# Optimization experiments

Hardware: AMD Instinct MI355X
Metric: run time of the kernel (lower is better)

## Reference

```python
import jax, jax.numpy as jnp
import numpy as np

EPS = 1e-8

def mlp(x, w1, b1, w2, b2):
    return jnp.tanh(x @ w1 + b1) @ w2 + b2

def setup_inputs() -> dict:
    key = jax.random.key(0)
    ks = jax.random.split(key, 24)
    N_NEWS, N_USERS, N_ATR = 50000, 100000, 1000
    E_ATR, E_USR = 100000, 2000000
    D = 768
    def lin(k, fi, fo):
        return jax.random.normal(k, (fi, fo), jnp.float32) * (1.0 / np.sqrt(fi))
    inp = {
        'news_x': jax.random.normal(ks[0], (N_NEWS, D), jnp.float32),
        'users_x': jax.random.normal(ks[1], (N_USERS, 128), jnp.float32),
        'w1a': lin(ks[2], D, 256), 'b1a': jnp.zeros((256,), jnp.float32),
        'w1b': lin(ks[3], 256, 128), 'b1b': jnp.zeros((128,), jnp.float32),
        'wna': lin(ks[4], D + 128, 512), 'bna': jnp.zeros((512,), jnp.float32),
        'wnb': lin(ks[5], 512, 128), 'bnb': jnp.zeros((128,), jnp.float32),
        'wua': lin(ks[6], 256, 256), 'bua': jnp.zeros((256,), jnp.float32),
        'wub': lin(ks[7], 256, 128), 'bub': jnp.zeros((128,), jnp.float32),
        'atr_row': jax.random.randint(ks[8], (E_ATR,), 0, N_NEWS, jnp.int32),
        'atr_col': jax.random.randint(ks[9], (E_ATR,), 0, N_ATR, jnp.int32),
        'usr_row': jax.random.randint(ks[10], (E_USR,), 0, N_NEWS, jnp.int32),
        'usr_col': jax.random.randint(ks[11], (E_USR,), 0, N_USERS, jnp.int32),
        'n_news': N_NEWS, 'n_users': N_USERS, 'n_atr': N_ATR,
    }
    return inp

def reference(news_x, users_x, w1a, b1a, w1b, b1b, wna, bna, wnb, bnb,
              wua, bua, wub, bub, atr_row, atr_col, usr_row, usr_col,
              n_news, n_users, n_atr):
    dt = news_x.dtype
    ones_a = jnp.ones(atr_row.shape[0], dt)
    ones_u = jnp.ones(usr_row.shape[0], dt)
    # FirstConv: news -> attribute nodes (edge_index.t() @ news)
    deg_atr = jax.ops.segment_sum(ones_a, atr_col, num_segments=n_atr)
    agr_atr = jax.ops.segment_sum(news_x[atr_row], atr_col, num_segments=n_atr)
    agr_atr = agr_atr / (deg_atr[:, None] + EPS)
    atr_feats = mlp(agr_atr, w1a, b1a, w1b, b1b)  # [n_atr, 128]
    # NewsConv: attribute -> news (edge_index @ atr_feats), concat with news_x
    deg_news = jax.ops.segment_sum(ones_a, atr_row, num_segments=n_news)
    agr_news = jax.ops.segment_sum(atr_feats[atr_col], atr_row, num_segments=n_news)
    agr_news = agr_news / (deg_news[:, None] + EPS)
    news_out = mlp(jnp.concatenate([news_x, agr_news], axis=1), wna, bna, wnb, bnb)  # [n_news,128]
    # UserConv: news -> users (edge_index['users'].t() @ news), concat with users_x
    deg_usr = jax.ops.segment_sum(ones_u, usr_col, num_segments=n_users)
    agr_usr = jax.ops.segment_sum(news_out[usr_row], usr_col, num_segments=n_users)
    agr_usr = agr_usr / (deg_usr[:, None] + EPS)
    users_out = mlp(jnp.concatenate([users_x, agr_usr], axis=1), wua, bua, wub, bub)  # [n_users,128]
    # stack final news + user embeddings into one array
    return jnp.concatenate([news_out, users_out], axis=0)  # [n_news+n_users, 128]
```

## Files before the change

### kernel.cpp

```cpp
#include <hip/hip_runtime.h>

#define N_NEWS 50000
#define N_USERS 100000
#define N_ATR 1000
#define E_ATR 100000
#define E_USR 2000000
#define EPSF 1e-8f

#define ACAP 192
#define NCAP 24
#define P_USR 250
#define UPP 400
#define ACAPP 9216
#define EBLK_A 4096

typedef short s16x8 __attribute__((ext_vector_type(8)));
typedef float f32x4 __attribute__((ext_vector_type(4)));

__device__ inline ushort f2bf(float f) {
    uint u = __float_as_uint(f);
    u += 0x7fffu + ((u >> 16) & 1u);
    return (ushort)(u >> 16);
}
__device__ inline float bflo(uint v) { return __uint_as_float(v << 16); }
__device__ inline float bfhi(uint v) { return __uint_as_float(v & 0xffff0000u); }
__device__ inline float fast_tanh(float x) {
    x = fminf(fmaxf(x, -15.0f), 15.0f);
    float e = __expf(2.0f * x);
    return (e - 1.0f) / (e + 1.0f);
}

struct TrJob { const float* src; ushort* dst; int R, C, blkEnd; };

struct PrepArgs {
    const int *atr_row, *atr_col, *usr_row, *usr_col;
    int *cnt_atr, *cnt_news, *arena_cnt;
    int *ids_atr, *ids_news;
    unsigned long long* arena;
    const float *news_x, *users_x;
    ushort *news_bf, *users_bf;
    int pa, fa, tr, n1, n2;
    TrJob j[6];
};

__global__ void prep_k(PrepArgs A) {
    __shared__ float tile[32][33];
    __shared__ int cloc[256], cscn[256], sexc[256], cbase[256];
    __shared__ ushort stageI[EBLK_A];
    int b = blockIdx.x;
    int t = threadIdx.x;
    if (b < A.pa) {
        cloc[t] = 0;
        __syncthreads();
        int base = b * EBLK_A;
        int endE = base + EBLK_A; if (endE > E_USR) endE = E_USR;
        int n = endE - base;
        for (int e = base + t; e < endE; e += 256)
            atomicAdd(&cloc[A.usr_col[e] / UPP], 1);
        __syncthreads();
        cscn[t] = cloc[t];
        __syncthreads();
        for (int off = 1; off < 256; off <<= 1) {
            int v = (t >= off) ? cscn[t - off] : 0;
            __syncthreads();
            cscn[t] += v;
            __syncthreads();
        }
        sexc[t] = cscn[t] - cloc[t];
        if (t < P_USR) cbase[t] = atomicAdd(&A.arena_cnt[t], cloc[t]);
        cloc[t] = 0;
        __syncthreads();
        for (int e = base + t; e < endE; e += 256) {
            int p = A.usr_col[e] / UPP;
            int off = atomicAdd(&cloc[p], 1);
            stageI[sexc[p] + off] = (ushort)(e - base);
        }
        __syncthreads();
        for (int i = t; i < n; i += 256) {
            int e = base + stageI[i];
            int c = A.usr_col[e];
            int r = A.usr_row[e];
            int p = c / UPP;
            int dst = cbase[p] + (i - sexc[p]);
            if (dst < ACAPP)
                A.arena[(size_t)p * ACAPP + dst] =
                    ((unsigned long long)(uint)c << 32) | (uint)r;
        }
        return;
    }
    b -= A.pa;
    if (b < A.fa) {
        int total = 2 * E_ATR;
        int per = (total + A.fa - 1) / A.fa;
        int base = b * per;
        int endE = base + per; if (endE > total) endE = total;
        for (int e = base + t; e < endE; e += 256) {
            if (e < E_ATR) {
                int c = A.atr_col[e];
                int slot = atomicAdd(&A.cnt_atr[c], 1);
                if (slot < ACAP) A.ids_atr[(size_t)c * ACAP + slot] = A.atr_row[e];
            } else {
                int e2 = e - E_ATR;
                int r = A.atr_row[e2];
                int slot = atomicAdd(&A.cnt_news[r], 1);
                if (slot < NCAP) A.ids_news[(size_t)r * NCAP + slot] = A.atr_col[e2];
            }
        }
        return;
    }
    b -= A.fa;
    if (b < A.tr) {
        int ji = 0;
        while (b >= A.j[ji].blkEnd) ++ji;
        const TrJob& J = A.j[ji];
        int lb = b - (ji ? A.j[ji - 1].blkEnd : 0);
        int ctiles = J.C / 32;
        int bc = (lb % ctiles) * 32, br = (lb / ctiles) * 32;
        int tx = t & 31, ty = t >> 5;
        for (int i = 0; i < 4; ++i)
            tile[ty + i * 8][tx] = J.src[(size_t)(br + ty + i * 8) * J.C + bc + tx];
        __syncthreads();
        for (int i = 0; i < 4; ++i)
            J.dst[(size_t)(bc + ty + i * 8) * J.R + br + tx] = f2bf(tile[tx][ty + i * 8]);
        return;
    }
    b -= A.tr;
    int i = b * 256 + t;
    const float* src; ushort* dst;
    if (i < A.n1) { src = A.news_x; dst = A.news_bf; }
    else          { i -= A.n1; if (i >= A.n2) return; src = A.users_x; dst = A.users_bf; }
    float4 a = ((const float4*)src)[i];
    uint2 v;
    v.x = (uint)f2bf(a.x) | ((uint)f2bf(a.y) << 16);
    v.y = (uint)f2bf(a.z) | ((uint)f2bf(a.w) << 16);
    ((uint2*)dst)[i] = v;
}

struct MidArgs {
    const unsigned long long* arena;
    const int* arena_cnt;
    int *cnt_usr, *start_usr, *ids_usr;
    const ushort* news_bf;
    const int* ids_atr;
    const int* cnt_atr;
    ushort* agr_atr_b;
};

__global__ void mid_k(MidArgs M) {
    __shared__ int cnt[512];
    __shared__ int scn[512];
    int b = blockIdx.x;
    int t = threadIdx.x;
    if (b < P_USR) {
        int p = b;
        int nA = M.arena_cnt[p]; if (nA > ACAPP) nA = ACAPP;
        const unsigned long long* ar = M.arena + (size_t)p * ACAPP;
        cnt[t] = 0; cnt[t + 256] = 0;
        __syncthreads();
        for (int i = t; i < nA; i += 256)
            atomicAdd(&cnt[(int)(ar[i] >> 32) - p * UPP], 1);
        __syncthreads();
        scn[t] = cnt[t]; scn[t + 256] = cnt[t + 256];
        __syncthreads();
        for (int off = 1; off < 512; off <<= 1) {
            int v0 = (t >= off) ? scn[t - off] : 0;
            int v1 = ((t + 256) >= off) ? scn[t + 256 - off] : 0;
            __syncthreads();
            scn[t] += v0; scn[t + 256] += v1;
            __syncthreads();
        }
        for (int i = t; i < UPP; i += 256) {
            int u = p * UPP + i;
            M.cnt_usr[u] = cnt[i];
            M.start_usr[u] = p * ACAPP + (scn[i] - cnt[i]);
        }
        __syncthreads();
        for (int i = t; i < UPP; i += 256) cnt[i] = scn[i] - cnt[i];
        __syncthreads();
        for (int i = t; i < nA; i += 256) {
            unsigned long long v = ar[i];
            int c = (int)(v >> 32);
            int off = atomicAdd(&cnt[c - p * UPP], 1);
            M.ids_usr[(size_t)p * ACAPP + off] = (int)(v & 0xffffffffu);
        }
        return;
    }
    b -= P_USR;
    int u = b;
    int dc = M.cnt_atr[u];
    int d = dc < ACAP ? dc : ACAP;
    const int* bp = M.ids_atr + (size_t)u * ACAP;
    const ushort* src = M.news_bf;
    float a0 = 0.f, a1 = 0.f, a2 = 0.f, a3 = 0.f;
    int i = 0;
    for (; i + 3 < d; i += 4) {
        const uint* r0 = (const uint*)(src + (size_t)bp[i] * 768);
        const uint* r1 = (const uint*)(src + (size_t)bp[i + 1] * 768);
        const uint* r2 = (const uint*)(src + (size_t)bp[i + 2] * 768);
        const uint* r3 = (const uint*)(src + (size_t)bp[i + 3] * 768);
        uint v0 = r0[t], v1 = r1[t], v2 = r2[t], v3 = r3[t];
        a0 += bflo(v0) + bflo(v1) + bflo(v2) + bflo(v3);
        a1 += bfhi(v0) + bfhi(v1) + bfhi(v2) + bfhi(v3);
        if (t < 128) {
            uint w0 = r0[t + 256], w1 = r1[t + 256], w2 = r2[t + 256], w3 = r3[t + 256];
            a2 += bflo(w0) + bflo(w1) + bflo(w2) + bflo(w3);
            a3 += bfhi(w0) + bfhi(w1) + bfhi(w2) + bfhi(w3);
        }
    }
    for (; i < d; ++i) {
        const uint* r0 = (const uint*)(src + (size_t)bp[i] * 768);
        uint v0 = r0[t];
        a0 += bflo(v0); a1 += bfhi(v0);
        if (t < 128) {
            uint v1 = r0[t + 256];
            a2 += bflo(v1); a3 += bfhi(v1);
        }
    }
    float inv = 1.0f / ((float)dc + EPSF);
    uint* dst = (uint*)(M.agr_atr_b + (size_t)u * 768);
    dst[t] = (uint)f2bf(a0 * inv) | ((uint)f2bf(a1 * inv) << 16);
    if (t < 128)
        dst[256 + t] = (uint)f2bf(a2 * inv) | ((uint)f2bf(a3 * inv) << 16);
}

template<int CAP>
__global__ void gather128c_k(const ushort* __restrict__ srcp, const int* __restrict__ ids,
                             const int* __restrict__ cnt, ushort* __restrict__ agr, int n) {
    int u = blockIdx.x * 8 + (threadIdx.x >> 5);
    if (u >= n) return;
    int lane = threadIdx.x & 31;
    int dc = cnt[u];
    int d = dc < CAP ? dc : CAP;
    const int* bp = ids + (size_t)u * CAP;
    float a0 = 0.f, a1 = 0.f, a2 = 0.f, a3 = 0.f;
    int i = 0;
    for (; i + 3 < d; i += 4) {
        int s0 = bp[i], s1 = bp[i + 1], s2 = bp[i + 2], s3 = bp[i + 3];
        uint2 v0 = *((const uint2*)(srcp + (size_t)s0 * 128) + lane);
        uint2 v1 = *((const uint2*)(srcp + (size_t)s1 * 128) + lane);
        uint2 v2 = *((const uint2*)(srcp + (size_t)s2 * 128) + lane);
        uint2 v3 = *((const uint2*)(srcp + (size_t)s3 * 128) + lane);
        a0 += bflo(v0.x) + bflo(v1.x) + bflo(v2.x) + bflo(v3.x);
        a1 += bfhi(v0.x) + bfhi(v1.x) + bfhi(v2.x) + bfhi(v3.x);
        a2 += bflo(v0.y) + bflo(v1.y) + bflo(v2.y) + bflo(v3.y);
        a3 += bfhi(v0.y) + bfhi(v1.y) + bfhi(v2.y) + bfhi(v3.y);
    }
    for (; i < d; ++i) {
        uint2 v0 = *((const uint2*)(srcp + (size_t)bp[i] * 128) + lane);
        a0 += bflo(v0.x); a1 += bfhi(v0.x);
        a2 += bflo(v0.y); a3 += bfhi(v0.y);
    }
    float inv = 1.0f / ((float)dc + EPSF);
    uint2 packed;
    packed.x = (uint)f2bf(a0 * inv) | ((uint)f2bf(a1 * inv) << 16);
    packed.y = (uint)f2bf(a2 * inv) | ((uint)f2bf(a3 * inv) << 16);
    *((uint2*)(agr + (size_t)u * 128) + lane) = packed;
}

__global__ void gather128s_k(const ushort* __restrict__ srcp, const int* __restrict__ ids,
                             const int* __restrict__ start, const int* __restrict__ cnt,
                             ushort* __restrict__ agr, int n) {
    int u = blockIdx.x * 8 + (threadIdx.x >> 5);
    if (u >= n) return;
    int lane = threadIdx.x & 31;
    int d = cnt[u];
    const int* bp = ids + start[u];
    float a0 = 0.f, a1 = 0.f, a2 = 0.f, a3 = 0.f;
    int i = 0;
    for (; i + 3 < d; i += 4) {
        int s0 = bp[i], s1 = bp[i + 1], s2 = bp[i + 2], s3 = bp[i + 3];
        uint2 v0 = *((const uint2*)(srcp + (size_t)s0 * 128) + lane);
        uint2 v1 = *((const uint2*)(srcp + (size_t)s1 * 128) + lane);
        uint2 v2 = *((const uint2*)(srcp + (size_t)s2 * 128) + lane);
        uint2 v3 = *((const uint2*)(srcp + (size_t)s3 * 128) + lane);
        a0 += bflo(v0.x) + bflo(v1.x) + bflo(v2.x) + bflo(v3.x);
        a1 += bfhi(v0.x) + bfhi(v1.x) + bfhi(v2.x) + bfhi(v3.x);
        a2 += bflo(v0.y) + bflo(v1.y) + bflo(v2.y) + bflo(v3.y);
        a3 += bfhi(v0.y) + bfhi(v1.y) + bfhi(v2.y) + bfhi(v3.y);
    }
    for (; i < d; ++i) {
        uint2 v0 = *((const uint2*)(srcp + (size_t)bp[i] * 128) + lane);
        a0 += bflo(v0.x); a1 += bfhi(v0.x);
        a2 += bflo(v0.y); a3 += bfhi(v0.y);
    }
    float inv = 1.0f / ((float)d + EPSF);
    uint2 packed;
    packed.x = (uint)f2bf(a0 * inv) | ((uint)f2bf(a1 * inv) << 16);
    packed.y = (uint)f2bf(a2 * inv) | ((uint)f2bf(a3 * inv) << 16);
    *((uint2*)(agr + (size_t)u * 128) + lane) = packed;
}

template<int NS, int NS1, bool TANH, int OMODE, int GY>
__launch_bounds__(256, 3)
__global__ void gemm5_k(const ushort* __restrict__ A1, const ushort* __restrict__ A2,
                        const ushort* __restrict__ Bt, const float* __restrict__ bias,
                        float* __restrict__ outf, ushort* __restrict__ outb,
                        int M, int N) {
    __shared__ __align__(16) char lds[32768];
    const int t = threadIdx.x;
    const int w = t >> 6, l = t & 63, lr = l & 15, lk = l >> 4;
    const int wm = w >> 1, wn = w & 1;
    int nwg = gridDim.x;
    int q = nwg >> 3, r = nwg & 7;
    int xcd = blockIdx.x & 7, idx = blockIdx.x >> 3;
    int fid = (xcd < r) ? xcd * (q + 1) + idx : r * (q + 1) + (xcd - r) * q + idx;
    constexpr int LG = (GY == 4) ? 2 : (GY == 2) ? 1 : 0;
    const int row0 = (fid >> LG) * 128;
    const int col0 = (fid & (GY - 1)) * 128;
    constexpr int A1RB = NS1 * 128;
    constexpr int A2RB = (NS - NS1) * 128;
    constexpr int BRB = NS * 128;

    auto stage = [&](int s) {
        const char* abase; int arb, soff;
        if (s < NS1) { abase = (const char*)A1; arb = A1RB; soff = s * 128; }
        else         { abase = (const char*)A2; arb = A2RB; soff = (s - NS1) * 128; }
#pragma unroll
        for (int i = 0; i < 4; ++i) {
            int chunk = i * 256 + w * 64 + l;
            int row = chunk >> 3, sub = chunk & 7;
            int rg = row0 + row; if (rg >= M) rg = M - 1;
            const char* src = abase + (size_t)rg * arb + soff + ((sub * 16) ^ ((row & 7) << 4));
            __builtin_amdgcn_global_load_lds(
                (const __attribute__((address_space(1))) unsigned int*)src,
                (__attribute__((address_space(3))) unsigned int*)(lds + i * 4096 + w * 1024),
                16, 0, 0);
        }
#pragma unroll
        for (int i = 0; i < 4; ++i) {
            int chunk = i * 256 + w * 64 + l;
            int row = chunk >> 3, sub = chunk & 7;
            const char* src = (const char*)Bt + (size_t)(col0 + row) * BRB + s * 128
                              + ((sub * 16) ^ ((row & 7) << 4));
            __builtin_amdgcn_global_load_lds(
                (const __attribute__((address_space(1))) unsigned int*)src,
                (__attribute__((address_space(3))) unsigned int*)(lds + 16384 + i * 4096 + w * 1024),
                16, 0, 0);
        }
    };

    f32x4 acc[4][4];
#pragma unroll
    for (int i = 0; i < 4; ++i)
#pragma unroll
        for (int j = 0; j < 4; ++j) acc[i][j] = (f32x4)0.f;

    stage(0);
    for (int s = 0; s < NS; ++s) {
        __syncthreads();
#pragma unroll
        for (int ks = 0; ks < 2; ++ks) {
            s16x8 af[4], bf[4];
#pragma unroll
            for (int rt = 0; rt < 4; ++rt) {
                int rr = wm * 64 + rt * 16 + lr;
                af[rt] = *(const s16x8*)(lds + rr * 128 + ((ks * 64 + lk * 16) ^ ((rr & 7) << 4)));
            }
#pragma unroll
            for (int ct = 0; ct < 4; ++ct) {
                int c = wn * 64 + ct * 16 + lr;
                bf[ct] = *(const s16x8*)(lds + 16384 + c * 128 + ((ks * 64 + lk * 16) ^ ((c & 7) << 4)));
            }
#pragma unroll
            for (int rt = 0; rt < 4; ++rt)
#pragma unroll
                for (int ct = 0; ct < 4; ++ct)
                    acc[rt][ct] = __builtin_amdgcn_mfma_f32_16x16x32_bf16(
                        af[rt], bf[ct], acc[rt][ct], 0, 0, 0);
        }
        __syncthreads();
        if (s + 1 < NS) stage(s + 1);
    }

    if (OMODE == 0) {
#pragma unroll
        for (int rt = 0; rt < 4; ++rt)
#pragma unroll
            for (int ct = 0; ct < 4; ++ct) {
                int c = wn * 64 + ct * 16 + lr;
                float bs = bias[col0 + c];
#pragma unroll
                for (int r4 = 0; r4 < 4; ++r4) {
                    int rr = wm * 64 + rt * 16 + lk * 4 + r4;
                    float v = acc[rt][ct][r4] + bs;
                    if (TANH) v = fast_tanh(v);
                    *(ushort*)(lds + rr * 256 + ((c * 2) ^ ((rr & 7) << 4))) = f2bf(v);
                }
            }
        __syncthreads();
#pragma unroll
        for (int i = 0; i < 8; ++i) {
            int chunk = i * 256 + t;
            int rr = chunk >> 4, cb = (chunk & 15) * 16;
            int rg = row0 + rr;
            if (rg < M)
                *(float4*)((char*)outb + (size_t)rg * (N * 2) + col0 * 2 + cb) =
                    *(const float4*)(lds + rr * 256 + (cb ^ ((rr & 7) << 4)));
        }
    } else {
#pragma unroll
        for (int rt = 0; rt < 4; ++rt)
#pragma unroll
            for (int ct = 0; ct < 4; ++ct) {
                int c = col0 + wn * 64 + ct * 16 + lr;
                float bs = bias[c];
#pragma unroll
                for (int r4 = 0; r4 < 4; ++r4) {
                    int rg = row0 + wm * 64 + rt * 16 + lk * 4 + r4;
                    if (rg < M) {
                        float v = acc[rt][ct][r4] + bs;
                        if (TANH) v = fast_tanh(v);
                        outf[(size_t)rg * N + c] = v;
                        if (OMODE == 2) outb[(size_t)rg * N + c] = f2bf(v);
                    }
                }
            }
    }
}

extern "C" void kernel_launch(void* const* d_in, const int* in_sizes, int n_in,
                              void* d_out, int out_size, void* d_ws, size_t ws_size,
                              hipStream_t stream) {
    const float* news_x  = (const float*)d_in[0];
    const float* users_x = (const float*)d_in[1];
    const float* w1a = (const float*)d_in[2];
    const float* b1a = (const float*)d_in[3];
    const float* w1b = (const float*)d_in[4];
    const float* b1b = (const float*)d_in[5];
    const float* wna = (const float*)d_in[6];
    const float* bna = (const float*)d_in[7];
    const float* wnb = (const float*)d_in[8];
    const float* bnb = (const float*)d_in[9];
    const float* wua = (const float*)d_in[10];
    const float* bua = (const float*)d_in[11];
    const float* wub = (const float*)d_in[12];
    const float* bub = (const float*)d_in[13];
    const int* atr_row = (const int*)d_in[14];
    const int* atr_col = (const int*)d_in[15];
    const int* usr_row = (const int*)d_in[16];
    const int* usr_col = (const int*)d_in[17];

    char* ws = (char*)d_ws;
    size_t o = 0;
    auto alloc = [&](size_t bytes) { void* p = ws + o; o += (bytes + 255) & ~(size_t)255; return p; };

    int* cnt_atr   = (int*)alloc(N_ATR * 4);
    int* cnt_news  = (int*)alloc(N_NEWS * 4);
    int* arena_cnt = (int*)alloc(P_USR * 4);
    size_t zero_bytes = o;
    int* cnt_usr   = (int*)alloc((size_t)N_USERS * 4);
    int* start_usr = (int*)alloc((size_t)N_USERS * 4);
    int* ids_atr  = (int*)alloc((size_t)N_ATR * ACAP * 4);
    int* ids_news = (int*)alloc((size_t)N_NEWS * NCAP * 4);
    int* ids_usr  = (int*)alloc((size_t)P_USR * ACAPP * 4);
    unsigned long long* arena = (unsigned long long*)alloc((size_t)P_USR * ACAPP * 8);
    ushort* news_bf    = (ushort*)alloc((size_t)N_NEWS * 768 * 2);
    ushort* users_bf   = (ushort*)alloc((size_t)N_USERS * 128 * 2);
    ushort* agr_atr_b  = (ushort*)alloc((size_t)N_ATR * 768 * 2);
    ushort* h_atr_b    = (ushort*)alloc((size_t)N_ATR * 256 * 2);
    ushort* atr_feats_b= (ushort*)alloc((size_t)N_ATR * 128 * 2);
    ushort* agr_news_b = (ushort*)alloc((size_t)N_NEWS * 128 * 2);
    ushort* agr_usr_b  = (ushort*)alloc((size_t)N_USERS * 128 * 2);
    ushort* out_news_b = (ushort*)alloc((size_t)N_NEWS * 128 * 2);
    ushort* h_buf      = (ushort*)alloc((size_t)N_USERS * 256 * 2);
    ushort* w1at = (ushort*)alloc((size_t)256 * 768 * 2);
    ushort* w1bt = (ushort*)alloc((size_t)128 * 256 * 2);
    ushort* wnat = (ushort*)alloc((size_t)512 * 896 * 2);
    ushort* wnbt = (ushort*)alloc((size_t)128 * 512 * 2);
    ushort* wuat = (ushort*)alloc((size_t)256 * 256 * 2);
    ushort* wubt = (ushort*)alloc((size_t)128 * 256 * 2);

    float* out = (float*)d_out;
    float* out_users = out + (size_t)N_NEWS * 128;

    hipMemsetAsync(cnt_atr, 0, zero_bytes, stream);

    {
        PrepArgs A;
        A.atr_row = atr_row; A.atr_col = atr_col;
        A.usr_row = usr_row; A.usr_col = usr_col;
        A.cnt_atr = cnt_atr; A.cnt_news = cnt_news; A.arena_cnt = arena_cnt;
        A.ids_atr = ids_atr; A.ids_news = ids_news;
        A.arena = arena;
        A.news_x = news_x; A.users_x = users_x;
        A.news_bf = news_bf; A.users_bf = users_bf;
        A.pa = (E_USR + EBLK_A - 1) / EBLK_A;
        A.fa = 25;
        A.n1 = N_NEWS * 768 / 4;
        A.n2 = N_USERS * 128 / 4;
        int acc2 = 0;
        auto add = [&](int i, const float* s, ushort* d, int R, int C) {
            acc2 += (C / 32) * (R / 32);
            A.j[i] = TrJob{s, d, R, C, acc2};
        };
        add(0, w1a, w1at, 768, 256);
        add(1, w1b, w1bt, 256, 128);
        add(2, wna, wnat, 896, 512);
        add(3, wnb, wnbt, 512, 128);
        add(4, wua, wuat, 256, 256);
        add(5, wub, wubt, 256, 128);
        A.tr = acc2;
        int cvt_blk = (A.n1 + A.n2 + 255) / 256;
        prep_k<<<A.pa + A.fa + A.tr + cvt_blk, 256, 0, stream>>>(A);
    }

    {
        MidArgs M;
        M.arena = arena; M.arena_cnt = arena_cnt;
        M.cnt_usr = cnt_usr; M.start_usr = start_usr; M.ids_usr = ids_usr;
        M.news_bf = news_bf; M.ids_atr = ids_atr; M.cnt_atr = cnt_atr;
        M.agr_atr_b = agr_atr_b;
        mid_k<<<P_USR + N_ATR, 256, 0, stream>>>(M);
    }

    gemm5_k<12, 12, true, 0, 2><<<16, 256, 0, stream>>>(
        agr_atr_b, nullptr, w1at, b1a, nullptr, h_atr_b, N_ATR, 256);
    gemm5_k<4, 4, false, 0, 1><<<8, 256, 0, stream>>>(
        h_atr_b, nullptr, w1bt, b1b, nullptr, atr_feats_b, N_ATR, 128);
    gather128c_k<NCAP><<<(N_NEWS + 7) / 8, 256, 0, stream>>>(
        atr_feats_b, ids_news, cnt_news, agr_news_b, N_NEWS);

    gemm5_k<14, 12, true, 0, 4><<<391 * 4, 256, 0, stream>>>(
        news_bf, agr_news_b, wnat, bna, nullptr, h_buf, N_NEWS, 512);
    gemm5_k<8, 8, false, 2, 1><<<391, 256, 0, stream>>>(
        h_buf, nullptr, wnbt, bnb, out, out_news_b, N_NEWS, 128);

    gather128s_k<<<(N_USERS + 7) / 8, 256, 0, stream>>>(
        out_news_b, ids_usr, start_usr, cnt_usr, agr_usr_b, N_USERS);
    gemm5_k<4, 2, true, 0, 2><<<782 * 2, 256, 0, stream>>>(
        users_bf, agr_usr_b, wuat, bua, nullptr, h_buf, N_USERS, 256);
    gemm5_k<4, 4, false, 1, 1><<<782, 256, 0, stream>>>(
        h_buf, nullptr, wubt, bub, out_users, nullptr, N_USERS, 128);
}
```

Baseline: 404.7 us.

## Fuse user MLP layers into one kernel keeping hidden tile in LDS

Replaces the two user-side GEMM launches with one fused kernel. Each block loads a 64-row tile of concatenated users_bf and agr_usr into LDS, computes the 256-wide tanh hidden layer with MFMA, writes it back to LDS as bf16, and then runs the second layer straight from LDS. This removes the write and reread of the 100000x256 hidden buffer through global memory and saves one launch. In exchange, weights are read directly from global memory per k-step rather than staged, and the tile shape is smaller.

```diff
diff --git a/kernel.cpp b/kernel.cpp
--- a/kernel.cpp
+++ b/kernel.cpp
@@ -418,6 +418,117 @@
     }
 }
 
+__launch_bounds__(256, 3)
+__global__ void mlp_users_fused(const ushort* __restrict__ users_bf,
+                                const ushort* __restrict__ agr_b,
+                                const ushort* __restrict__ wuat,
+                                const float* __restrict__ bua,
+                                const ushort* __restrict__ wubt,
+                                const float* __restrict__ bub,
+                                float* __restrict__ outf, int M) {
+    __shared__ __align__(16) char lds[32768];
+    const int t = threadIdx.x;
+    const int w = t >> 6, l = t & 63, lr = l & 15, lk = l >> 4;
+    const int row0 = blockIdx.x * 64;
+
+#pragma unroll
+    for (int i = 0; i < 8; ++i) {
+        int chunk = i * 256 + w * 64 + l;
+        int row = chunk >> 5;
+        int rg = row0 + row; if (rg >= M) rg = M - 1;
+        int off = ((chunk * 16) & 511) ^ ((row & 7) << 4);
+        int sc = off >> 4;
+        const char* src = (sc < 16)
+            ? (const char*)users_bf + (size_t)rg * 256 + sc * 16
+            : (const char*)agr_b + (size_t)rg * 256 + (sc - 16) * 16;
+        __builtin_amdgcn_global_load_lds(
+            (const __attribute__((address_space(1))) unsigned int*)src,
+            (__attribute__((address_space(3))) unsigned int*)(lds + i * 4096 + w * 1024),
+            16, 0, 0);
+    }
+    __syncthreads();
+
+    f32x4 acc[4][4];
+#pragma unroll
+    for (int i = 0; i < 4; ++i)
+#pragma unroll
+        for (int j = 0; j < 4; ++j) acc[i][j] = (f32x4)0.f;
+#pragma unroll
+    for (int ks = 0; ks < 8; ++ks) {
+        s16x8 af[4], bf[4];
+#pragma unroll
+        for (int rt = 0; rt < 4; ++rt) {
+            int rr = rt * 16 + lr;
+            af[rt] = *(const s16x8*)(lds + ((rr * 512 + ks * 64 + lk * 16) ^ ((rr & 7) << 4)));
+        }
+#pragma unroll
+        for (int ct = 0; ct < 4; ++ct) {
+            int c = w * 64 + ct * 16 + lr;
+            bf[ct] = *(const s16x8*)(wuat + (size_t)c * 256 + ks * 32 + lk * 8);
+        }
+#pragma unroll
+        for (int rt = 0; rt < 4; ++rt)
+#pragma unroll
+            for (int ct = 0; ct < 4; ++ct)
+                acc[rt][ct] = __builtin_amdgcn_mfma_f32_16x16x32_bf16(
+                    af[rt], bf[ct], acc[rt][ct], 0, 0, 0);
+    }
+    __syncthreads();
+
+#pragma unroll
+    for (int rt = 0; rt < 4; ++rt)
+#pragma unroll
+        for (int ct = 0; ct < 4; ++ct) {
+            int c = w * 64 + ct * 16 + lr;
+            float bs = bua[c];
+#pragma unroll
+            for (int r4 = 0; r4 < 4; ++r4) {
+                int rr = rt * 16 + lk * 4 + r4;
+                ushort h = f2bf(fast_tanh(acc[rt][ct][r4] + bs));
+                *(ushort*)(lds + ((rr * 512 + c * 2) ^ ((rr & 7) << 4))) = h;
+            }
+        }
+    __syncthreads();
+
+    f32x4 acc2[4][2];
+#pragma unroll
+    for (int i = 0; i < 4; ++i)
+#pragma unroll
+        for (int j = 0; j < 2; ++j) acc2[i][j] = (f32x4)0.f;
+#pragma unroll
+    for (int ks = 0; ks < 8; ++ks) {
+        s16x8 af[4], bf[2];
+#pragma unroll
+        for (int rt = 0; rt < 4; ++rt) {
+            int rr = rt * 16 + lr;
+            af[rt] = *(const s16x8*)(lds + ((rr * 512 + ks * 64 + lk * 16) ^ ((rr & 7) << 4)));
+        }
+#pragma unroll
+        for (int ct = 0; ct < 2; ++ct) {
+            int c = w * 32 + ct * 16 + lr;
+            bf[ct] = *(const s16x8*)(wubt + (size_t)c * 256 + ks * 32 + lk * 8);
+        }
+#pragma unroll
+        for (int rt = 0; rt < 4; ++rt)
+#pragma unroll
+            for (int ct = 0; ct < 2; ++ct)
+                acc2[rt][ct] = __builtin_amdgcn_mfma_f32_16x16x32_bf16(
+                    af[rt], bf[ct], acc2[rt][ct], 0, 0, 0);
+    }
+#pragma unroll
+    for (int rt = 0; rt < 4; ++rt)
+#pragma unroll
+        for (int ct = 0; ct < 2; ++ct) {
+            int c = w * 32 + ct * 16 + lr;
+            float bs = bub[c];
+#pragma unroll
+            for (int r4 = 0; r4 < 4; ++r4) {
+                int rg = row0 + rt * 16 + lk * 4 + r4;
+                if (rg < M) outf[(size_t)rg * 128 + c] = acc2[rt][ct][r4] + bs;
+            }
+        }
+}
+
 extern "C" void kernel_launch(void* const* d_in, const int* in_sizes, int n_in,
                               void* d_out, int out_size, void* d_ws, size_t ws_size,
                               hipStream_t stream) {
@@ -462,7 +573,7 @@
     ushort* agr_news_b = (ushort*)alloc((size_t)N_NEWS * 128 * 2);
     ushort* agr_usr_b  = (ushort*)alloc((size_t)N_USERS * 128 * 2);
     ushort* out_news_b = (ushort*)alloc((size_t)N_NEWS * 128 * 2);
-    ushort* h_buf      = (ushort*)alloc((size_t)N_USERS * 256 * 2);
+    ushort* h_buf      = (ushort*)alloc((size_t)N_NEWS * 512 * 2);
     ushort* w1at = (ushort*)alloc((size_t)256 * 768 * 2);
     ushort* w1bt = (ushort*)alloc((size_t)128 * 256 * 2);
     ushort* wnat = (ushort*)alloc((size_t)512 * 896 * 2);
@@ -527,8 +638,6 @@
 
     gather128s_k<<<(N_USERS + 7) / 8, 256, 0, stream>>>(
         out_news_b, ids_usr, start_usr, cnt_usr, agr_usr_b, N_USERS);
-    gemm5_k<4, 2, true, 0, 2><<<782 * 2, 256, 0, stream>>>(
-        users_bf, agr_usr_b, wuat, bua, nullptr, h_buf, N_USERS, 256);
-    gemm5_k<4, 4, false, 1, 1><<<782, 256, 0, stream>>>(
-        h_buf, nullptr, wubt, bub, out_users, nullptr, N_USERS, 128);
-}
+    mlp_users_fused<<<(N_USERS + 63) / 64, 256, 0, stream>>>(
+        users_bf, agr_usr_b, wuat, bua, wubt, bub, out_users, N_USERS);
+}
```

After: 407.7 us. Within noise of the previous version (+0.7%).
